# Optimization experiments

Measured on AMD Instinct MI355X. Metric: run time of the kernel, lower is better.

The kernel has to match this reference:

```python
import jax, jax.numpy as jnp
import numpy as np

B, L = 512, 256
N_NEG, L_NEG = 20, 64
VOCAB = 50000  # table has VOCAB+1 rows (row 0 = padding)
D = 100
K = 14
LAMBDA = 1.0


def setup_inputs() -> dict:
    key = jax.random.key(0)
    k1, k2, k3, k4, k5, k6, k7, k8 = jax.random.split(key, 8)
    pos_ids = jax.random.randint(k1, (B, L), 0, VOCAB + 1)
    neg_ids = jax.random.randint(k2, (B, N_NEG, L_NEG), 0, VOCAB + 1)
    emb_table = jax.random.normal(k3, (VOCAB + 1, D), dtype=jnp.float32) * 0.1
    emb_table = emb_table.at[0].set(0.0)  # padding row is zeros
    W_att = jax.random.normal(k4, (D, D), dtype=jnp.float32) * 0.05
    Wk = jax.random.normal(k5, (D, K), dtype=jnp.float32) * 0.1
    bk = jnp.zeros((K,), dtype=jnp.float32)
    Wf = jax.random.normal(k6, (K, D), dtype=jnp.float32) * 0.1  # aspect matrix (kmeans-init in original)
    bf = jnp.zeros((D,), dtype=jnp.float32)
    return {"pos_ids": pos_ids, "neg_ids": neg_ids, "emb_table": emb_table,
            "W_att": W_att, "Wk": Wk, "bk": bk, "Wf": Wf, "bf": bf}


def reference(pos_ids, neg_ids, emb_table, W_att, Wk, bk, Wf, bf):
    mask = pos_ids != 0                                   # [B, L]
    maskf = mask.astype(jnp.float32)
    e = emb_table[pos_ids]                                # [B, L, D]
    # --- masked aspect attention ---
    ys = jnp.mean(e, axis=-2)                             # [B, D] (unmasked mean, as in source)
    eW = jnp.einsum('bld,de->ble', e, W_att) * maskf[..., None]
    f = jnp.einsum('bld,bd->bl', eW, ys)[..., None]       # [B, L, 1]
    f = f + ((~mask).astype(f.dtype) * -1e9)[..., None]
    att = jax.nn.softmax(f, axis=-2)                      # softmax over L
    zs = jnp.sum(att * e, axis=-2)                        # [B, D]
    # --- aspect probabilities and reconstruction ---
    pt = jax.nn.sigmoid(zs @ Wk + bk)                     # [B, K]
    rs = pt @ Wf + bf                                     # [B, D]
    # --- orthogonality reg (faithful to source: uses the NORMS, normalize(...)[1]) ---
    norms = jnp.linalg.norm(Wf, axis=1, keepdims=True)    # [K, 1]
    reg = norms @ norms.T - jnp.ones((K, K), dtype=jnp.float32)
    reg = jnp.sqrt(jnp.sum(reg * reg))                    # Frobenius norm
    # --- margin loss ---
    pos_term = jnp.sum(rs * zs)                           # tensordot(rs, zs, [[0,1],[0,1]])
    a = jnp.mean(emb_table[neg_ids], axis=-2)             # [B, N_NEG, D]
    # tensordot(a, expand_dims(rs,-2), [[0,2],[0,2]]) -> [N_NEG, 1], then reduce_sum
    neg_term = jnp.sum(jnp.einsum('bnd,bd->n', a, rs))
    loss = jax.nn.relu(1.0 - neg_term + pos_term) + LAMBDA * reg
    return (loss, pt, rs)
```

## Files before the change

kernel.cpp:

```cpp
#include <hip/hip_runtime.h>
#include <hip/hip_bf16.h>

#if !__has_builtin(__builtin_amdgcn_cvt_pk_f32_fp8) || !__has_builtin(__builtin_amdgcn_cvt_pk_fp8_f32)
#include <hip/hip_fp8.h>
#endif

#define Bx 512
#define Lx 256
#define Dx 100
#define Kx 14
#define VROWS 50001
#define NEG_ROWS 1280
#define NEG_CHUNKS 5
#define NEG_CHUNK 256
#define NBLK_ATTN Bx
#define NBLK_NEG (Bx * NEG_CHUNKS)
#define ACC_N (4 + Bx * Dx)

#define PAD8  128
#define RAW8  100

typedef float floatx2 __attribute__((ext_vector_type(2)));

__device__ __forceinline__ float dot4(float4 a, float4 b) {
    return a.x * b.x + a.y * b.y + a.z * b.z + a.w * b.w;
}

__device__ __forceinline__ float4 fp8x4_dec(unsigned u) {
#if __has_builtin(__builtin_amdgcn_cvt_pk_f32_fp8)
    floatx2 lo = __builtin_amdgcn_cvt_pk_f32_fp8((int)u, false);
    floatx2 hi = __builtin_amdgcn_cvt_pk_f32_fp8((int)u, true);
    return make_float4(lo.x, lo.y, hi.x, hi.y);
#else
    __hip_fp8_e4m3 a, b, c, d;
    a.__x = (unsigned char)(u & 0xFF);
    b.__x = (unsigned char)((u >> 8) & 0xFF);
    c.__x = (unsigned char)((u >> 16) & 0xFF);
    d.__x = (unsigned char)((u >> 24) & 0xFF);
    return make_float4((float)a, (float)b, (float)c, (float)d);
#endif
}

__device__ __forceinline__ unsigned fp8x4_enc(float4 v) {
#if __has_builtin(__builtin_amdgcn_cvt_pk_fp8_f32)
    int p = 0;
    p = __builtin_amdgcn_cvt_pk_fp8_f32(v.x, v.y, p, false);
    p = __builtin_amdgcn_cvt_pk_fp8_f32(v.z, v.w, p, true);
    return (unsigned)p;
#else
    __hip_fp8_e4m3 a(v.x), b(v.y), c(v.z), d(v.w);
    return (unsigned)a.__x | ((unsigned)b.__x << 8) |
           ((unsigned)c.__x << 16) | ((unsigned)d.__x << 24);
#endif
}

__global__ __launch_bounds__(256) void convert_kernel(
    const float* __restrict__ table, unsigned char* __restrict__ tb8,
    float* __restrict__ acc, int RS8, int padded)
{
    const int gid = blockIdx.x * 256 + threadIdx.x;
    if (gid < ACC_N) acc[gid] = 0.0f;
    const int row = gid >> 5;
    const int c   = gid & 31;
    if (row >= VROWS) return;
    if (c < 25) {
        const float4 v = *reinterpret_cast<const float4*>(
            table + (size_t)row * Dx + c * 4);
        *reinterpret_cast<unsigned*>(tb8 + (size_t)row * RS8 + c * 4) = fp8x4_enc(v);
    } else if (padded) {
        *reinterpret_cast<unsigned*>(tb8 + (size_t)row * RS8 + c * 4) = 0u;
    }
}

__global__ __launch_bounds__(256) void fused_gather(
    const int* __restrict__ pos_ids, const int* __restrict__ neg_ids,
    const unsigned char* __restrict__ tb8,
    const float* __restrict__ W_att, const float* __restrict__ Wk,
    const float* __restrict__ bk, const float* __restrict__ Wf,
    const float* __restrict__ bf, float* __restrict__ pt_out,
    float* __restrict__ rs_out, float* __restrict__ acc, float* __restrict__ g,
    int RS8)
{
    const int tid  = threadIdx.x;
    const int grp  = tid >> 5;
    const int lane = tid & 31;
    const int bid  = blockIdx.x;

    __shared__ __align__(16) float4 part4[8][26];
    __shared__ int   ids[Lx];
    __shared__ float red[Lx];
    __shared__ __align__(16) float ys_sh[104];
    __shared__ __align__(16) float t_sh[104];
    __shared__ float zs_sh[104];
    __shared__ float pt_sh[Kx];
    __shared__ float m_sh[8], s_sh[8], sc_sh[8];

    float* pf = (float*)part4;

    if (bid >= NBLK_ATTN) {
        const int j = bid - NBLK_ATTN;
        const int b = j / NEG_CHUNKS;
        const int c = j - b * NEG_CHUNKS;
        const int* idp = neg_ids + (size_t)b * NEG_ROWS + c * NEG_CHUNK;

        ids[tid] = idp[tid];
        __syncthreads();

        if (lane < 25) {
            const int o = lane * 4;
            float4 a0 = {0,0,0,0}, a1 = {0,0,0,0}, a2 = {0,0,0,0}, a3 = {0,0,0,0};
            for (int r = grp; r < NEG_CHUNK; r += 32) {
                const unsigned u0 = *(const unsigned*)(tb8 + (size_t)ids[r]      * RS8 + o);
                const unsigned u1 = *(const unsigned*)(tb8 + (size_t)ids[r + 8]  * RS8 + o);
                const unsigned u2 = *(const unsigned*)(tb8 + (size_t)ids[r + 16] * RS8 + o);
                const unsigned u3 = *(const unsigned*)(tb8 + (size_t)ids[r + 24] * RS8 + o);
                const float4 v0 = fp8x4_dec(u0);
                const float4 v1 = fp8x4_dec(u1);
                const float4 v2 = fp8x4_dec(u2);
                const float4 v3 = fp8x4_dec(u3);
                a0.x += v0.x; a0.y += v0.y; a0.z += v0.z; a0.w += v0.w;
                a1.x += v1.x; a1.y += v1.y; a1.z += v1.z; a1.w += v1.w;
                a2.x += v2.x; a2.y += v2.y; a2.z += v2.z; a2.w += v2.w;
                a3.x += v3.x; a3.y += v3.y; a3.z += v3.z; a3.w += v3.w;
            }
            a0.x += a1.x + a2.x + a3.x; a0.y += a1.y + a2.y + a3.y;
            a0.z += a1.z + a2.z + a3.z; a0.w += a1.w + a2.w + a3.w;
            part4[grp][lane] = a0;
        }
        __syncthreads();
        if (tid < Dx) {
            float s = 0.f;
            #pragma unroll
            for (int gg = 0; gg < 8; ++gg) s += pf[gg * 104 + tid];
            atomicAdd(&g[(size_t)b * Dx + tid], s);
        }
        return;
    }

    const int b = bid;
    ids[tid] = pos_ids[(size_t)b * Lx + tid];
    __syncthreads();

    if (lane < 25) {
        const int o = lane * 4;
        float4 a0 = {0,0,0,0}, a1 = {0,0,0,0}, a2 = {0,0,0,0}, a3 = {0,0,0,0};
        for (int r = grp; r < Lx; r += 32) {
            const float4 v0 = fp8x4_dec(*(const unsigned*)(tb8 + (size_t)ids[r]      * RS8 + o));
            const float4 v1 = fp8x4_dec(*(const unsigned*)(tb8 + (size_t)ids[r + 8]  * RS8 + o));
            const float4 v2 = fp8x4_dec(*(const unsigned*)(tb8 + (size_t)ids[r + 16] * RS8 + o));
            const float4 v3 = fp8x4_dec(*(const unsigned*)(tb8 + (size_t)ids[r + 24] * RS8 + o));
            a0.x += v0.x; a0.y += v0.y; a0.z += v0.z; a0.w += v0.w;
            a1.x += v1.x; a1.y += v1.y; a1.z += v1.z; a1.w += v1.w;
            a2.x += v2.x; a2.y += v2.y; a2.z += v2.z; a2.w += v2.w;
            a3.x += v3.x; a3.y += v3.y; a3.z += v3.z; a3.w += v3.w;
        }
        a0.x += a1.x + a2.x + a3.x; a0.y += a1.y + a2.y + a3.y;
        a0.z += a1.z + a2.z + a3.z; a0.w += a1.w + a2.w + a3.w;
        part4[grp][lane] = a0;
    }
    __syncthreads();
    if (tid < Dx) {
        float s = 0.f;
        #pragma unroll
        for (int gg = 0; gg < 8; ++gg) s += pf[gg * 104 + tid];
        ys_sh[tid] = s * (1.0f / Lx);
    }
    __syncthreads();

    if (tid < Dx) {
        const float* wrow = W_att + (size_t)tid * Dx;
        float s = 0.f;
        #pragma unroll 4
        for (int e = 0; e < Dx; ++e) s += wrow[e] * ys_sh[e];
        t_sh[tid] = s;
    }
    if (tid >= Dx && tid < 104) t_sh[tid] = 0.f;
    __syncthreads();

    {
        const float4 tl = (lane < 25) ? ((const float4*)t_sh)[lane]
                                      : make_float4(0.f, 0.f, 0.f, 0.f);
        float m = -1e30f, ssum = 0.f;
        float4 za = {0.f, 0.f, 0.f, 0.f};
        for (int r = grp; r < Lx; r += 16) {
            const int id0 = ids[r];
            const int id1 = ids[r + 8];
            float4 e0 = {0,0,0,0}, e1 = {0,0,0,0};
            if (lane < 25) {
                e0 = fp8x4_dec(*(const unsigned*)(tb8 + (size_t)id0 * RS8 + lane * 4));
                e1 = fp8x4_dec(*(const unsigned*)(tb8 + (size_t)id1 * RS8 + lane * 4));
            }
            float d0 = dot4(e0, tl);
            float d1 = dot4(e1, tl);
            #pragma unroll
            for (int o = 16; o > 0; o >>= 1) {
                d0 += __shfl_xor(d0, o, 32);
                d1 += __shfl_xor(d1, o, 32);
            }
            const float f0 = (id0 != 0) ? d0 : -1e30f;
            const float f1 = (id1 != 0) ? d1 : -1e30f;
            const float mn = fmaxf(m, fmaxf(f0, f1));
            const float sc = expf(m - mn);
            const float w0 = (id0 != 0) ? expf(d0 - mn) : 0.f;
            const float w1 = (id1 != 0) ? expf(d1 - mn) : 0.f;
            ssum = ssum * sc + w0 + w1;
            za.x = za.x * sc + w0 * e0.x + w1 * e1.x;
            za.y = za.y * sc + w0 * e0.y + w1 * e1.y;
            za.z = za.z * sc + w0 * e0.z + w1 * e1.z;
            za.w = za.w * sc + w0 * e0.w + w1 * e1.w;
            m = mn;
        }
        if (lane == 0) { m_sh[grp] = m; s_sh[grp] = ssum; }
        if (lane < 25) part4[grp][lane] = za;
    }
    __syncthreads();
    if (tid < 8) {
        float M = -1e30f;
        #pragma unroll
        for (int gg = 0; gg < 8; ++gg) M = fmaxf(M, m_sh[gg]);
        sc_sh[tid] = expf(m_sh[tid] - M);
    }
    __syncthreads();
    if (tid < Dx) {
        float S = 0.f, z = 0.f;
        #pragma unroll
        for (int gg = 0; gg < 8; ++gg) {
            S += s_sh[gg] * sc_sh[gg];
            z += pf[gg * 104 + tid] * sc_sh[gg];
        }
        zs_sh[tid] = z / S;
    }
    __syncthreads();

    if (tid < Kx) {
        float s = bk[tid];
        for (int d = 0; d < Dx; ++d) s += zs_sh[d] * Wk[d * Kx + tid];
        const float pk = 1.0f / (1.0f + expf(-s));
        pt_sh[tid] = pk;
        pt_out[(size_t)b * Kx + tid] = pk;
    }
    __syncthreads();

    float contrib = 0.f;
    if (tid < Dx) {
        float r = bf[tid];
        #pragma unroll
        for (int k = 0; k < Kx; ++k) r += pt_sh[k] * Wf[k * Dx + tid];
        rs_out[(size_t)b * Dx + tid] = r;
        contrib = r * zs_sh[tid];
    }
    red[tid] = contrib;
    __syncthreads();
    for (int s = 128; s > 0; s >>= 1) {
        if (tid < s) red[tid] += red[tid + s];
        __syncthreads();
    }
    if (tid == 0) atomicAdd(&acc[0], red[0]);
}

__global__ __launch_bounds__(1024) void loss_kernel(
    const float* __restrict__ Wf, const float* __restrict__ acc,
    const float* __restrict__ g, const float* __restrict__ rs,
    float* __restrict__ out)
{
    __shared__ float n[Kx];
    __shared__ float red[1024];
    const int tid = threadIdx.x;

    float v = 0.f;
    for (int i = tid; i < Bx * Dx; i += 1024) v += g[i] * rs[i];
    red[tid] = v;
    __syncthreads();
    for (int s = 512; s > 0; s >>= 1) {
        if (tid < s) red[tid] += red[tid + s];
        __syncthreads();
    }
    const float neg_term = red[0] * (1.0f / 64.0f);
    __syncthreads();

    if (tid < Kx) {
        float s = 0.f;
        for (int d = 0; d < Dx; ++d) {
            const float w = Wf[tid * Dx + d];
            s += w * w;
        }
        n[tid] = sqrtf(s);
    }
    __syncthreads();

    float vv = 0.f;
    if (tid < Kx * Kx) {
        const int i = tid / Kx;
        const int j = tid - i * Kx;
        const float x = n[i] * n[j] - 1.0f;
        vv = x * x;
    }
    red[tid] = vv;
    __syncthreads();
    for (int s = 512; s > 0; s >>= 1) {
        if (tid < s) red[tid] += red[tid + s];
        __syncthreads();
    }
    if (tid == 0) {
        const float reg = sqrtf(red[0]);
        const float margin = 1.0f - neg_term + acc[0];
        out[0] = fmaxf(margin, 0.0f) + reg;
    }
}

extern "C" void kernel_launch(void* const* d_in, const int* in_sizes, int n_in,
                              void* d_out, int out_size, void* d_ws, size_t ws_size,
                              hipStream_t stream) {
    const int*   pos_ids = (const int*)  d_in[0];
    const int*   neg_ids = (const int*)  d_in[1];
    const float* table   = (const float*)d_in[2];
    const float* W_att   = (const float*)d_in[3];
    const float* Wk      = (const float*)d_in[4];
    const float* bk      = (const float*)d_in[5];
    const float* Wf      = (const float*)d_in[6];
    const float* bf      = (const float*)d_in[7];

    float* out    = (float*)d_out;
    float* pt_out = out + 1;
    float* rs_out = out + 1 + (size_t)Bx * Kx;

    const size_t need_pad = (size_t)VROWS * PAD8 + 16 + (size_t)ACC_N * 4;
    const int padded = (ws_size >= need_pad) ? 1 : 0;
    const int RS8 = padded ? PAD8 : RAW8;

    unsigned char* tb8 = (unsigned char*)d_ws;
    size_t acc_off = (size_t)VROWS * RS8;
    acc_off = (acc_off + 15) & ~(size_t)15;
    float* acc = (float*)((char*)d_ws + acc_off);
    float* g   = acc + 4;

    const int nthreads = VROWS * 32;
    convert_kernel<<<(nthreads + 255) / 256, 256, 0, stream>>>(
        table, tb8, acc, RS8, padded);
    fused_gather<<<NBLK_ATTN + NBLK_NEG, 256, 0, stream>>>(
        pos_ids, neg_ids, tb8, W_att, Wk, bk, Wf, bf,
        pt_out, rs_out, acc, g, RS8);
    loss_kernel<<<1, 1024, 0, stream>>>(Wf, acc, g, rs_out, out);
}
```

Before: 136.0 us.

## Fuse negative gather and final loss into one per-batch kernel with last-block reduction

```diff
diff --git a/kernel.cpp b/kernel.cpp
--- a/kernel.cpp
+++ b/kernel.cpp
@@ -11,11 +11,8 @@
 #define Kx 14
 #define VROWS 50001
 #define NEG_ROWS 1280
-#define NEG_CHUNKS 5
-#define NEG_CHUNK 256
-#define NBLK_ATTN Bx
-#define NBLK_NEG (Bx * NEG_CHUNKS)
-#define ACC_N (4 + Bx * Dx)
+#define TPB 512
+#define NGRP 16
 
 #define PAD8  128
 #define RAW8  100
@@ -56,104 +53,125 @@
 
 __global__ __launch_bounds__(256) void convert_kernel(
     const float* __restrict__ table, unsigned char* __restrict__ tb8,
-    float* __restrict__ acc, int RS8, int padded)
+    const float* __restrict__ Wf, float* __restrict__ acc, int RS8, int padded)
 {
-    const int gid = blockIdx.x * 256 + threadIdx.x;
-    if (gid < ACC_N) acc[gid] = 0.0f;
+    const int tid = threadIdx.x;
+    const int gid = blockIdx.x * 256 + tid;
+    if (gid < 4) acc[gid] = 0.0f;
+
     const int row = gid >> 5;
     const int c   = gid & 31;
-    if (row >= VROWS) return;
-    if (c < 25) {
-        const float4 v = *reinterpret_cast<const float4*>(
-            table + (size_t)row * Dx + c * 4);
-        *reinterpret_cast<unsigned*>(tb8 + (size_t)row * RS8 + c * 4) = fp8x4_enc(v);
-    } else if (padded) {
-        *reinterpret_cast<unsigned*>(tb8 + (size_t)row * RS8 + c * 4) = 0u;
-    }
-}
-
-__global__ __launch_bounds__(256) void fused_gather(
+    if (row < VROWS) {
+        if (c < 25) {
+            const float4 v = *reinterpret_cast<const float4*>(
+                table + (size_t)row * Dx + c * 4);
+            *reinterpret_cast<unsigned*>(tb8 + (size_t)row * RS8 + c * 4) = fp8x4_enc(v);
+        } else if (padded) {
+            *reinterpret_cast<unsigned*>(tb8 + (size_t)row * RS8 + c * 4) = 0u;
+        }
+    }
+
+    if (blockIdx.x == 0) {
+        __shared__ float n_sh[Kx];
+        __shared__ float r_sh[256];
+        if (tid < Kx) {
+            const float4* w4 = reinterpret_cast<const float4*>(Wf + (size_t)tid * Dx);
+            float s = 0.f;
+            #pragma unroll
+            for (int i = 0; i < 25; ++i) { const float4 w = w4[i]; s += dot4(w, w); }
+            n_sh[tid] = sqrtf(s);
+        }
+        __syncthreads();
+        float vv = 0.f;
+        if (tid < Kx * Kx) {
+            const int i = tid / Kx;
+            const int j = tid - i * Kx;
+            const float x = n_sh[i] * n_sh[j] - 1.0f;
+            vv = x * x;
+        }
+        r_sh[tid] = vv;
+        __syncthreads();
+        for (int s = 128; s > 0; s >>= 1) {
+            if (tid < s) r_sh[tid] += r_sh[tid + s];
+            __syncthreads();
+        }
+        if (tid == 0) acc[3] = sqrtf(r_sh[0]);
+    }
+}
+
+__global__ __launch_bounds__(TPB) void fused_all(
     const int* __restrict__ pos_ids, const int* __restrict__ neg_ids,
     const unsigned char* __restrict__ tb8,
     const float* __restrict__ W_att, const float* __restrict__ Wk,
     const float* __restrict__ bk, const float* __restrict__ Wf,
     const float* __restrict__ bf, float* __restrict__ pt_out,
-    float* __restrict__ rs_out, float* __restrict__ acc, float* __restrict__ g,
-    int RS8)
+    float* __restrict__ rs_out, float* __restrict__ acc,
+    float* __restrict__ out, int RS8)
 {
     const int tid  = threadIdx.x;
     const int grp  = tid >> 5;
     const int lane = tid & 31;
-    const int bid  = blockIdx.x;
-
-    __shared__ __align__(16) float4 part4[8][26];
+    const int b    = blockIdx.x;
+
+    __shared__ __align__(16) unsigned rowbuf[Lx][26];
     __shared__ int   ids[Lx];
-    __shared__ float red[Lx];
+    __shared__ int   idn[NEG_ROWS];
+    __shared__ __align__(16) float4 part4[NGRP][26];
     __shared__ __align__(16) float ys_sh[104];
     __shared__ __align__(16) float t_sh[104];
     __shared__ float zs_sh[104];
     __shared__ float pt_sh[Kx];
-    __shared__ float m_sh[8], s_sh[8], sc_sh[8];
+    __shared__ float m_sh[NGRP], s_sh[NGRP], sc_sh[NGRP];
+    __shared__ float wred[8][2];
 
     float* pf = (float*)part4;
 
-    if (bid >= NBLK_ATTN) {
-        const int j = bid - NBLK_ATTN;
-        const int b = j / NEG_CHUNKS;
-        const int c = j - b * NEG_CHUNKS;
-        const int* idp = neg_ids + (size_t)b * NEG_ROWS + c * NEG_CHUNK;
-
-        ids[tid] = idp[tid];
-        __syncthreads();
-
-        if (lane < 25) {
-            const int o = lane * 4;
-            float4 a0 = {0,0,0,0}, a1 = {0,0,0,0}, a2 = {0,0,0,0}, a3 = {0,0,0,0};
-            for (int r = grp; r < NEG_CHUNK; r += 32) {
-                const unsigned u0 = *(const unsigned*)(tb8 + (size_t)ids[r]      * RS8 + o);
-                const unsigned u1 = *(const unsigned*)(tb8 + (size_t)ids[r + 8]  * RS8 + o);
-                const unsigned u2 = *(const unsigned*)(tb8 + (size_t)ids[r + 16] * RS8 + o);
-                const unsigned u3 = *(const unsigned*)(tb8 + (size_t)ids[r + 24] * RS8 + o);
-                const float4 v0 = fp8x4_dec(u0);
-                const float4 v1 = fp8x4_dec(u1);
-                const float4 v2 = fp8x4_dec(u2);
-                const float4 v3 = fp8x4_dec(u3);
-                a0.x += v0.x; a0.y += v0.y; a0.z += v0.z; a0.w += v0.w;
-                a1.x += v1.x; a1.y += v1.y; a1.z += v1.z; a1.w += v1.w;
-                a2.x += v2.x; a2.y += v2.y; a2.z += v2.z; a2.w += v2.w;
-                a3.x += v3.x; a3.y += v3.y; a3.z += v3.z; a3.w += v3.w;
-            }
-            a0.x += a1.x + a2.x + a3.x; a0.y += a1.y + a2.y + a3.y;
-            a0.z += a1.z + a2.z + a3.z; a0.w += a1.w + a2.w + a3.w;
-            part4[grp][lane] = a0;
-        }
-        __syncthreads();
-        if (tid < Dx) {
-            float s = 0.f;
-            #pragma unroll
-            for (int gg = 0; gg < 8; ++gg) s += pf[gg * 104 + tid];
-            atomicAdd(&g[(size_t)b * Dx + tid], s);
-        }
-        return;
-    }
-
-    const int b = bid;
-    ids[tid] = pos_ids[(size_t)b * Lx + tid];
-    __syncthreads();
-
+    if (tid < Lx) ids[tid] = pos_ids[(size_t)b * Lx + tid] * RS8;
+    for (int i = tid; i < NEG_ROWS; i += TPB)
+        idn[i] = neg_ids[(size_t)b * NEG_ROWS + i] * RS8;
+    __syncthreads();
+
+    float4 na = {0.f, 0.f, 0.f, 0.f};
     if (lane < 25) {
         const int o = lane * 4;
         float4 a0 = {0,0,0,0}, a1 = {0,0,0,0}, a2 = {0,0,0,0}, a3 = {0,0,0,0};
-        for (int r = grp; r < Lx; r += 32) {
-            const float4 v0 = fp8x4_dec(*(const unsigned*)(tb8 + (size_t)ids[r]      * RS8 + o));
-            const float4 v1 = fp8x4_dec(*(const unsigned*)(tb8 + (size_t)ids[r + 8]  * RS8 + o));
-            const float4 v2 = fp8x4_dec(*(const unsigned*)(tb8 + (size_t)ids[r + 16] * RS8 + o));
-            const float4 v3 = fp8x4_dec(*(const unsigned*)(tb8 + (size_t)ids[r + 24] * RS8 + o));
+        for (int r = grp; r < NEG_ROWS; r += 64) {
+            const float4 v0 = fp8x4_dec(*(const unsigned*)(tb8 + (size_t)idn[r]      + o));
+            const float4 v1 = fp8x4_dec(*(const unsigned*)(tb8 + (size_t)idn[r + 16] + o));
+            const float4 v2 = fp8x4_dec(*(const unsigned*)(tb8 + (size_t)idn[r + 32] + o));
+            const float4 v3 = fp8x4_dec(*(const unsigned*)(tb8 + (size_t)idn[r + 48] + o));
             a0.x += v0.x; a0.y += v0.y; a0.z += v0.z; a0.w += v0.w;
             a1.x += v1.x; a1.y += v1.y; a1.z += v1.z; a1.w += v1.w;
             a2.x += v2.x; a2.y += v2.y; a2.z += v2.z; a2.w += v2.w;
             a3.x += v3.x; a3.y += v3.y; a3.z += v3.z; a3.w += v3.w;
         }
+        na.x = a0.x + a1.x + a2.x + a3.x;
+        na.y = a0.y + a1.y + a2.y + a3.y;
+        na.z = a0.z + a1.z + a2.z + a3.z;
+        na.w = a0.w + a1.w + a2.w + a3.w;
+    }
+
+    if (lane < 25) {
+        const int o = lane * 4;
+        float4 a0 = {0,0,0,0}, a1 = {0,0,0,0}, a2 = {0,0,0,0}, a3 = {0,0,0,0};
+        for (int r = grp; r < Lx; r += 64) {
+            const unsigned u0 = *(const unsigned*)(tb8 + (size_t)ids[r]      + o);
+            const unsigned u1 = *(const unsigned*)(tb8 + (size_t)ids[r + 16] + o);
+            const unsigned u2 = *(const unsigned*)(tb8 + (size_t)ids[r + 32] + o);
+            const unsigned u3 = *(const unsigned*)(tb8 + (size_t)ids[r + 48] + o);
+            rowbuf[r][lane]      = u0;
+            rowbuf[r + 16][lane] = u1;
+            rowbuf[r + 32][lane] = u2;
+            rowbuf[r + 48][lane] = u3;
+            const float4 v0 = fp8x4_dec(u0);
+            const float4 v1 = fp8x4_dec(u1);
+            const float4 v2 = fp8x4_dec(u2);
+            const float4 v3 = fp8x4_dec(u3);
+            a0.x += v0.x; a0.y += v0.y; a0.z += v0.z; a0.w += v0.w;
+            a1.x += v1.x; a1.y += v1.y; a1.z += v1.z; a1.w += v1.w;
+            a2.x += v2.x; a2.y += v2.y; a2.z += v2.z; a2.w += v2.w;
+            a3.x += v3.x; a3.y += v3.y; a3.z += v3.z; a3.w += v3.w;
+        }
         a0.x += a1.x + a2.x + a3.x; a0.y += a1.y + a2.y + a3.y;
         a0.z += a1.z + a2.z + a3.z; a0.w += a1.w + a2.w + a3.w;
         part4[grp][lane] = a0;
@@ -162,19 +180,19 @@
     if (tid < Dx) {
         float s = 0.f;
         #pragma unroll
-        for (int gg = 0; gg < 8; ++gg) s += pf[gg * 104 + tid];
+        for (int g = 0; g < NGRP; ++g) s += pf[g * 104 + tid];
         ys_sh[tid] = s * (1.0f / Lx);
     }
     __syncthreads();
 
     if (tid < Dx) {
-        const float* wrow = W_att + (size_t)tid * Dx;
+        const float4* w4 = reinterpret_cast<const float4*>(W_att + (size_t)tid * Dx);
+        const float4* y4 = reinterpret_cast<const float4*>(ys_sh);
         float s = 0.f;
-        #pragma unroll 4
-        for (int e = 0; e < Dx; ++e) s += wrow[e] * ys_sh[e];
+        #pragma unroll
+        for (int i = 0; i < 25; ++i) s += dot4(w4[i], y4[i]);
         t_sh[tid] = s;
     }
-    if (tid >= Dx && tid < 104) t_sh[tid] = 0.f;
     __syncthreads();
 
     {
@@ -182,13 +200,13 @@
                                       : make_float4(0.f, 0.f, 0.f, 0.f);
         float m = -1e30f, ssum = 0.f;
         float4 za = {0.f, 0.f, 0.f, 0.f};
-        for (int r = grp; r < Lx; r += 16) {
+        for (int r = grp; r < Lx; r += 32) {
             const int id0 = ids[r];
-            const int id1 = ids[r + 8];
+            const int id1 = ids[r + 16];
             float4 e0 = {0,0,0,0}, e1 = {0,0,0,0};
             if (lane < 25) {
-                e0 = fp8x4_dec(*(const unsigned*)(tb8 + (size_t)id0 * RS8 + lane * 4));
-                e1 = fp8x4_dec(*(const unsigned*)(tb8 + (size_t)id1 * RS8 + lane * 4));
+                e0 = fp8x4_dec(rowbuf[r][lane]);
+                e1 = fp8x4_dec(rowbuf[r + 16][lane]);
             }
             float d0 = dot4(e0, tl);
             float d1 = dot4(e1, tl);
@@ -214,19 +232,19 @@
         if (lane < 25) part4[grp][lane] = za;
     }
     __syncthreads();
-    if (tid < 8) {
+    if (tid < NGRP) {
         float M = -1e30f;
         #pragma unroll
-        for (int gg = 0; gg < 8; ++gg) M = fmaxf(M, m_sh[gg]);
+        for (int g = 0; g < NGRP; ++g) M = fmaxf(M, m_sh[g]);
         sc_sh[tid] = expf(m_sh[tid] - M);
     }
     __syncthreads();
     if (tid < Dx) {
         float S = 0.f, z = 0.f;
         #pragma unroll
-        for (int gg = 0; gg < 8; ++gg) {
-            S += s_sh[gg] * sc_sh[gg];
-            z += pf[gg * 104 + tid] * sc_sh[gg];
+        for (int g = 0; g < NGRP; ++g) {
+            S += s_sh[g] * sc_sh[g];
+            z += pf[g * 104 + tid] * sc_sh[g];
         }
         zs_sh[tid] = z / S;
     }
@@ -241,70 +259,49 @@
     }
     __syncthreads();
 
-    float contrib = 0.f;
+    float posc = 0.f, negc = 0.f, rs_reg = 0.f;
     if (tid < Dx) {
         float r = bf[tid];
         #pragma unroll
         for (int k = 0; k < Kx; ++k) r += pt_sh[k] * Wf[k * Dx + tid];
         rs_out[(size_t)b * Dx + tid] = r;
-        contrib = r * zs_sh[tid];
-    }
-    red[tid] = contrib;
-    __syncthreads();
-    for (int s = 128; s > 0; s >>= 1) {
-        if (tid < s) red[tid] += red[tid + s];
-        __syncthreads();
-    }
-    if (tid == 0) atomicAdd(&acc[0], red[0]);
-}
-
-__global__ __launch_bounds__(1024) void loss_kernel(
-    const float* __restrict__ Wf, const float* __restrict__ acc,
-    const float* __restrict__ g, const float* __restrict__ rs,
-    float* __restrict__ out)
-{
-    __shared__ float n[Kx];
-    __shared__ float red[1024];
-    const int tid = threadIdx.x;
-
-    float v = 0.f;
-    for (int i = tid; i < Bx * Dx; i += 1024) v += g[i] * rs[i];
-    red[tid] = v;
-    __syncthreads();
-    for (int s = 512; s > 0; s >>= 1) {
-        if (tid < s) red[tid] += red[tid + s];
-        __syncthreads();
-    }
-    const float neg_term = red[0] * (1.0f / 64.0f);
-    __syncthreads();
-
-    if (tid < Kx) {
-        float s = 0.f;
-        for (int d = 0; d < Dx; ++d) {
-            const float w = Wf[tid * Dx + d];
-            s += w * w;
-        }
-        n[tid] = sqrtf(s);
-    }
-    __syncthreads();
-
-    float vv = 0.f;
-    if (tid < Kx * Kx) {
-        const int i = tid / Kx;
-        const int j = tid - i * Kx;
-        const float x = n[i] * n[j] - 1.0f;
-        vv = x * x;
-    }
-    red[tid] = vv;
-    __syncthreads();
-    for (int s = 512; s > 0; s >>= 1) {
-        if (tid < s) red[tid] += red[tid + s];
-        __syncthreads();
-    }
+        rs_reg = r;
+        posc = r * zs_sh[tid];
+    }
+
+    if (lane < 25) part4[grp][lane] = na;
+    __syncthreads();
+    if (tid < Dx) {
+        float gsum = 0.f;
+        #pragma unroll
+        for (int g = 0; g < NGRP; ++g) gsum += pf[g * 104 + tid];
+        negc = gsum * rs_reg;
+    }
+
+    #pragma unroll
+    for (int o = 32; o > 0; o >>= 1) {
+        posc += __shfl_xor(posc, o);
+        negc += __shfl_xor(negc, o);
+    }
+    const int wid = tid >> 6;
+    if ((tid & 63) == 0) { wred[wid][0] = posc; wred[wid][1] = negc; }
+    __syncthreads();
+
     if (tid == 0) {
-        const float reg = sqrtf(red[0]);
-        const float margin = 1.0f - neg_term + acc[0];
-        out[0] = fmaxf(margin, 0.0f) + reg;
+        float P = 0.f, N = 0.f;
+        #pragma unroll
+        for (int w = 0; w < 8; ++w) { P += wred[w][0]; N += wred[w][1]; }
+        atomicAdd(&acc[0], P);
+        atomicAdd(&acc[1], N);
+        __threadfence();
+        const unsigned t = atomicAdd(reinterpret_cast<unsigned int*>(acc) + 2, 1u);
+        if (t == (unsigned)(Bx - 1)) {
+            const float pos = atomicAdd(&acc[0], 0.0f);
+            const float neg = atomicAdd(&acc[1], 0.0f);
+            const float reg = atomicAdd(&acc[3], 0.0f);
+            const float margin = 1.0f - neg * (1.0f / 64.0f) + pos;
+            out[0] = fmaxf(margin, 0.0f) + reg;
+        }
     }
 }
 
@@ -324,7 +321,7 @@
     float* pt_out = out + 1;
     float* rs_out = out + 1 + (size_t)Bx * Kx;
 
-    const size_t need_pad = (size_t)VROWS * PAD8 + 16 + (size_t)ACC_N * 4;
+    const size_t need_pad = (size_t)VROWS * PAD8 + 16 + 4 * sizeof(float);
     const int padded = (ws_size >= need_pad) ? 1 : 0;
     const int RS8 = padded ? PAD8 : RAW8;
 
@@ -332,13 +329,11 @@
     size_t acc_off = (size_t)VROWS * RS8;
     acc_off = (acc_off + 15) & ~(size_t)15;
     float* acc = (float*)((char*)d_ws + acc_off);
-    float* g   = acc + 4;
 
     const int nthreads = VROWS * 32;
     convert_kernel<<<(nthreads + 255) / 256, 256, 0, stream>>>(
-        table, tb8, acc, RS8, padded);
-    fused_gather<<<NBLK_ATTN + NBLK_NEG, 256, 0, stream>>>(
+        table, tb8, Wf, acc, RS8, padded);
+    fused_all<<<Bx, TPB, 0, stream>>>(
         pos_ids, neg_ids, tb8, W_att, Wk, bk, Wf, bf,
-        pt_out, rs_out, acc, g, RS8);
-    loss_kernel<<<1, 1024, 0, stream>>>(Wf, acc, g, rs_out, out);
-}
+        pt_out, rs_out, acc, out, RS8);
+}
```

Measured after the change: 128.6 us. -5.4%, faster.
